# Kernel optimization log

Hardware: AMD Instinct MI355X
Metric: run time of the kernel (lower is better)

Reference implementation:

```python
import jax, jax.numpy as jnp
import numpy as np

H = 1024        # hidden_size
M = 1024        # memory_size
NH = 16         # num_heads
DH = H // NH    # head_dim
CR = 4          # compression_ratio
B, S = 4, 2048


def _lin(x, W, b):
    return x @ W + b


def setup_inputs() -> dict:
    key = jax.random.key(0)
    ks = iter(jax.random.split(key, 32))
    p = lambda *shape: jax.random.normal(next(ks), shape, dtype=jnp.float32) * 0.02
    inp = {
        'hidden_states': jax.random.normal(next(ks), (B, S, H), dtype=jnp.float32),
        'memory_bank': jax.random.normal(next(ks), (B, M, H), dtype=jnp.float32),
        'memory_mask': jnp.ones((B, M), dtype=bool),
        'write_pointer': 700,
        # compressor: Linear(H*CR -> H), SiLU, Linear(H -> H)
        'Wc1': p(H * CR, H), 'bc1': jnp.zeros((H,), jnp.float32),
        'Wc2': p(H, H), 'bc2': jnp.zeros((H,), jnp.float32),
        # attention projections
        'Wq': p(H, H), 'bq': jnp.zeros((H,), jnp.float32),
        'Wk': p(H, H), 'bk': jnp.zeros((H,), jnp.float32),
        'Wv': p(H, H), 'bv': jnp.zeros((H,), jnp.float32),
        'Wo': p(H, H), 'bo': jnp.zeros((H,), jnp.float32),
        # write gate: Linear(H -> H//2), SiLU, Linear(H//2 -> 1), Sigmoid
        'Wwg1': p(H, H // 2), 'bwg1': jnp.zeros((H // 2,), jnp.float32),
        'Wwg2': p(H // 2, 1), 'bwg2': jnp.zeros((1,), jnp.float32),
        # read gate: Linear(2H -> H//2), SiLU, Linear(H//2 -> 1), Sigmoid
        'Wrg1': p(2 * H, H // 2), 'brg1': jnp.zeros((H // 2,), jnp.float32),
        'Wrg2': p(H // 2, 1), 'brg2': jnp.zeros((1,), jnp.float32),
        # LayerNorm
        'ln_g': jnp.ones((H,), jnp.float32), 'ln_b': jnp.zeros((H,), jnp.float32),
    }
    return inp


def _forward(hidden_states, memory_bank, memory_mask, write_pointer,
             Wc1, bc1, Wc2, bc2, Wq, bq, Wk, bk, Wv, bv, Wo, bo,
             Wwg1, bwg1, Wwg2, bwg2, Wrg1, brg1, Wrg2, brg2, ln_g, ln_b):
    # ---- memory attention ----
    q = _lin(hidden_states, Wq, bq).reshape(B, S, NH, DH)
    k = _lin(memory_bank, Wk, bk).reshape(B, M, NH, DH)
    v = _lin(memory_bank, Wv, bv).reshape(B, M, NH, DH)
    scale = DH ** -0.5
    scores = jnp.einsum('bqhd,bkhd->bhqk', q, k) * scale
    scores = jnp.where(memory_mask[:, None, None, :], scores, -jnp.inf)
    probs = jnp.nan_to_num(jax.nn.softmax(scores, axis=-1), nan=0.0)
    retrieved = jnp.einsum('bhqk,bkhd->bqhd', probs, v).reshape(B, S, H)
    retrieved = _lin(retrieved, Wo, bo)

    # ---- read gate + residual + layernorm ----
    gate_in = jnp.concatenate([hidden_states, retrieved], axis=-1)
    rg = jax.nn.sigmoid(_lin(jax.nn.silu(_lin(gate_in, Wrg1, brg1)), Wrg2, brg2))
    out = hidden_states + rg * retrieved
    mu = jnp.mean(out, axis=-1, keepdims=True)
    var = jnp.var(out, axis=-1, keepdims=True)
    out = (out - mu) * jax.lax.rsqrt(var + 1e-5) * ln_g + ln_b

    # ---- write to memory ----
    wg = jax.nn.sigmoid(_lin(jax.nn.silu(_lin(hidden_states, Wwg1, bwg1)), Wwg2, bwg2))  # [B,S,1]
    L = S // CR  # S divisible by CR -> no padding needed (pad path is a no-op)
    compressed = _lin(jax.nn.silu(_lin(hidden_states.reshape(B, L, CR * H), Wc1, bc1)), Wc2, bc2)
    wg = wg.reshape(B, L, CR, 1).mean(axis=2)
    gated = compressed * wg  # [B,L,H]

    idx = (write_pointer + jnp.arange(L)) % M  # circular-buffer indices (unique since L <= M)
    new_bank = memory_bank.at[:, idx].set(gated)
    new_mask = memory_mask.at[:, idx].set(True)
    new_ptr = (write_pointer + L) % M
    return out, new_bank, new_mask, new_ptr


def reference(hidden_states, memory_bank, memory_mask, write_pointer,
              Wc1, bc1, Wc2, bc2, Wq, bq, Wk, bk, Wv, bv, Wo, bo,
              Wwg1, bwg1, Wwg2, bwg2, Wrg1, brg1, Wrg2, brg2, ln_g, ln_b):
    return _forward(hidden_states, memory_bank, memory_mask, write_pointer,
                    Wc1, bc1, Wc2, bc2, Wq, bq, Wk, bk, Wv, bv, Wo, bo,
                    Wwg1, bwg1, Wwg2, bwg2, Wrg1, brg1, Wrg2, brg2, ln_g, ln_b)
```

## Files before the change

kernel.cpp:

```cpp
#include <hip/hip_runtime.h>
#include <hip/hip_bf16.h>

#define Bb 4
#define Ss 2048
#define Hh 1024
#define Mm 1024
#define NHh 16
#define DHh 64
#define CRr 4
#define Ll (Ss / CRr)

#define SC2 0.18033688f

typedef __attribute__((ext_vector_type(8))) short short8;
typedef __attribute__((ext_vector_type(4))) float f32x4;
typedef __attribute__((ext_vector_type(16))) float f32x16;

typedef __attribute__((address_space(1))) const unsigned int g_u32;
typedef __attribute__((address_space(3))) unsigned int l_u32;

__device__ inline void gload_lds16(const void* g, void* l) {
    __builtin_amdgcn_global_load_lds((g_u32*)g, (l_u32*)l, 16, 0, 0);
}

__device__ inline unsigned short f2bf(float x) {
    unsigned int u = __builtin_bit_cast(unsigned int, x);
    unsigned int r = u + 0x7FFFu + ((u >> 16) & 1u);
    return (unsigned short)(r >> 16);
}
__device__ inline float bf2f(unsigned short u) {
    return __builtin_bit_cast(float, (unsigned int)u << 16);
}
__device__ inline unsigned int cvtpk_bf16(float lo, float hi2) {
    unsigned int r;
    asm("v_cvt_pk_bf16_f32 %0, %1, %2" : "=v"(r) : "v"(lo), "v"(hi2));
    return r;
}
__device__ inline f32x16 zero16() {
    f32x16 v;
    #pragma unroll
    for (int i = 0; i < 16; ++i) v[i] = 0.0f;
    return v;
}
__device__ inline short8 lds_frag(const unsigned short* base, int row, int slot) {
    return *(const short8*)((const char*)base + row * 128 + ((slot ^ (row & 7)) << 4));
}

#define N8_HS  (Bb * Ss * Hh / 8)
#define N8_BK  (Bb * Mm * Hh / 8)
__global__ __launch_bounds__(256) void cast2_kernel(
    const float* __restrict__ hs, const float* __restrict__ bank,
    unsigned short* __restrict__ hs_bf, unsigned short* __restrict__ bank_bf)
{
    int i = blockIdx.x * 256 + threadIdx.x;
    const float* src; unsigned short* dst;
    if (i < N8_HS) { src = hs; dst = hs_bf; }
    else           { src = bank; dst = bank_bf; i -= N8_HS; if (i >= N8_BK) return; }
    const float4* p = reinterpret_cast<const float4*>(src) + (size_t)i * 2;
    float4 a = p[0], b = p[1];
    uint4 o;
    o.x = (unsigned)f2bf(a.x) | ((unsigned)f2bf(a.y) << 16);
    o.y = (unsigned)f2bf(a.z) | ((unsigned)f2bf(a.w) << 16);
    o.z = (unsigned)f2bf(b.x) | ((unsigned)f2bf(b.y) << 16);
    o.w = (unsigned)f2bf(b.z) | ((unsigned)f2bf(b.w) << 16);
    *reinterpret_cast<uint4*>(dst + (size_t)i * 8) = o;
}

__global__ __launch_bounds__(256) void transpose_all_kernel(
    const float* __restrict__ Wq, const float* __restrict__ Wwg1,
    const float* __restrict__ Wk, const float* __restrict__ Wv,
    const float* __restrict__ Wo, const float* __restrict__ Wrg1,
    const float* __restrict__ Wc1, const float* __restrict__ Wc2,
    unsigned short* wtQW, unsigned short* wtKV, unsigned short* wtO,
    unsigned short* wtRG, unsigned short* wtC1, unsigned short* wtC2)
{
    int bid = blockIdx.x;
    const float* src; unsigned short* dst; int K, N;
    if (bid < 1024)      { src = Wq;   dst = wtQW;              K = 1024; N = 1024; }
    else if (bid < 1536) { src = Wwg1; dst = wtQW + 1048576;    K = 1024; N = 512;  bid -= 1024; }
    else if (bid < 2560) { src = Wk;   dst = wtKV;              K = 1024; N = 1024; bid -= 1536; }
    else if (bid < 3584) { src = Wv;   dst = wtKV + 1048576;    K = 1024; N = 1024; bid -= 2560; }
    else if (bid < 4608) { src = Wo;   dst = wtO;               K = 1024; N = 1024; bid -= 3584; }
    else if (bid < 5632) { src = Wrg1; dst = wtRG;              K = 2048; N = 512;  bid -= 4608; }
    else if (bid < 9728) { src = Wc1;  dst = wtC1;              K = 4096; N = 1024; bid -= 5632; }
    else                 { src = Wc2;  dst = wtC2;              K = 1024; N = 1024; bid -= 9728; }
    const int ntx = N >> 5;
    const int k0 = (bid / ntx) * 32, n0 = (bid % ntx) * 32;

    __shared__ float tile[32][33];
    const int tx = threadIdx.x & 31, ty = threadIdx.x >> 5;
    #pragma unroll
    for (int r = 0; r < 32; r += 8)
        tile[r + ty][tx] = src[(size_t)(k0 + r + ty) * N + n0 + tx];
    __syncthreads();
    #pragma unroll
    for (int r = 0; r < 32; r += 8)
        dst[(size_t)(n0 + r + ty) * K + k0 + tx] = f2bf(tile[tx][r + ty]);
}

__global__ void maskbias_kernel(const unsigned char* __restrict__ mask,
                                float* __restrict__ bias_arr)
{
    const int i = blockIdx.x * 256 + threadIdx.x;
    if (i < Bb * Mm) bias_arr[i] = mask[i] ? 0.0f : -1.0e30f;
}

#define GM_BF16  0
#define GM_BF16S 1
#define GM_BF16T 2
#define GM_F32G  3

__global__ __launch_bounds__(256) void gemm_bf16_kernel(
    const unsigned short* __restrict__ A1, const unsigned short* __restrict__ A2,
    int K1, const unsigned short* __restrict__ Wt,
    const float* __restrict__ bias1, const float* __restrict__ bias2, int N1,
    void* out1, void* out2, int mode1, int mode2,
    int Mdim, int Ntot, int Kdim,
    const int* __restrict__ wp_ptr, const float* __restrict__ wg_row)
{
    __shared__ __align__(16) unsigned short As[128 * 64];
    __shared__ __align__(16) unsigned short Bs[128 * 64];

    const int t = threadIdx.x;
    const int l = t & 63;
    const int w = t >> 6;

    const int nx = gridDim.x;
    const int nwg = nx * gridDim.y;
    const int bid0 = blockIdx.y * nx + blockIdx.x;
    const int swz = (nwg & 7) ? bid0 : ((bid0 & 7) * (nwg >> 3) + (bid0 >> 3));
    const int bm = (swz / nx) * 128;
    const int bn = (swz % nx) * 128;

    const int m_off = (w >> 1) * 64;
    const int n_off = (w & 1) * 64;
    const int K2 = Kdim - K1;

    f32x4 acc[4][4];
    const f32x4 z = {0.f, 0.f, 0.f, 0.f};
    #pragma unroll
    for (int i = 0; i < 4; ++i)
        #pragma unroll
        for (int j = 0; j < 4; ++j) acc[i][j] = z;

    for (int kt = 0; kt < Kdim; kt += 64) {
        __syncthreads();
        const unsigned short* Ap; int rsA, kl;
        if (kt < K1) { Ap = A1; rsA = K1; kl = kt; }
        else         { Ap = A2; rsA = K2; kl = kt - K1; }
        #pragma unroll
        for (int i = 0; i < 4; ++i) {
            const int c = i * 256 + t;
            const int row = c >> 3;
            const int p = (c & 7) ^ (row & 7);
            gload_lds16(Ap + (size_t)(bm + row) * rsA + kl + p * 8,
                        (char*)As + c * 16);
            gload_lds16(Wt + (size_t)(bn + row) * Kdim + kt + p * 8,
                        (char*)Bs + c * 16);
        }
        __syncthreads();
        #pragma unroll
        for (int kk = 0; kk < 2; ++kk) {
            short8 af[4], bfr[4];
            #pragma unroll
            for (int i = 0; i < 4; ++i) {
                af[i]  = lds_frag(As, m_off + i * 16 + (l & 15), kk * 4 + (l >> 4));
                bfr[i] = lds_frag(Bs, n_off + i * 16 + (l & 15), kk * 4 + (l >> 4));
            }
            #pragma unroll
            for (int i = 0; i < 4; ++i)
                #pragma unroll
                for (int j = 0; j < 4; ++j)
                    acc[i][j] = __builtin_amdgcn_mfma_f32_16x16x32_bf16(
                        af[i], bfr[j], acc[i][j], 0, 0, 0);
        }
    }

    float gg[16]; int wpv = 0;
    if (mode1 == GM_F32G) {
        wpv = *wp_ptr;
        #pragma unroll
        for (int i = 0; i < 4; ++i)
            #pragma unroll
            for (int r = 0; r < 4; ++r) {
                const int row = bm + m_off + i * 16 + (l >> 4) * 4 + r;
                gg[i * 4 + r] = 0.25f * (wg_row[4 * row] + wg_row[4 * row + 1] +
                                         wg_row[4 * row + 2] + wg_row[4 * row + 3]);
            }
    }

    #pragma unroll
    for (int j = 0; j < 4; ++j) {
        const int col = bn + n_off + j * 16 + (l & 15);
        const bool sec = (col >= N1);
        const int cl = sec ? col - N1 : col;
        const int mode = sec ? mode2 : mode1;
        const float bj = sec ? bias2[cl] : bias1[cl];
        const int nd = sec ? (Ntot - N1) : N1;
        if (mode == GM_BF16T) {
            unsigned short* ob = (unsigned short*)out2;
            #pragma unroll
            for (int i = 0; i < 4; ++i) {
                const int row0 = bm + m_off + i * 16 + (l >> 4) * 4;
                const int bidx = row0 >> 10, key = row0 & 1023;
                ushort4 pk4;
                pk4.x = f2bf(acc[i][j][0] + bj);
                pk4.y = f2bf(acc[i][j][1] + bj);
                pk4.z = f2bf(acc[i][j][2] + bj);
                pk4.w = f2bf(acc[i][j][3] + bj);
                *(ushort4*)(ob + ((size_t)bidx << 20) + (size_t)cl * 1024 + key) = pk4;
            }
        } else if (mode == GM_F32G) {
            float* ob = (float*)out1;
            #pragma unroll
            for (int i = 0; i < 4; ++i)
                #pragma unroll
                for (int r = 0; r < 4; ++r) {
                    const int row = bm + m_off + i * 16 + (l >> 4) * 4 + r;
                    const int bb = row >> 9, lx = row & 511;
                    const int m = (wpv + lx) & 1023;
                    ob[((size_t)(bb * 1024 + m)) * 1024 + col] =
                        (acc[i][j][r] + bj) * gg[i * 4 + r];
                }
        } else {
            unsigned short* ob = (unsigned short*)(sec ? out2 : out1);
            #pragma unroll
            for (int i = 0; i < 4; ++i)
                #pragma unroll
                for (int r = 0; r < 4; ++r) {
                    const int row = bm + m_off + i * 16 + (l >> 4) * 4 + r;
                    float v0 = acc[i][j][r] + bj;
                    if (mode == GM_BF16S) v0 = v0 / (1.0f + __expf(-v0));
                    ob[(size_t)row * nd + cl] = f2bf(v0);
                }
        }
    }
}

__global__ __launch_bounds__(256) void attn_mfma_kernel(
    const unsigned short* __restrict__ q, const unsigned short* __restrict__ k,
    const unsigned short* __restrict__ vt, const float* __restrict__ bias_arr,
    unsigned short* __restrict__ out)
{
    const int qt = blockIdx.x, h = blockIdx.y, b = blockIdx.z;
    const int t = threadIdx.x, l = t & 63, w = t >> 6;
    const int lq = l & 31, hi = l >> 5;

    __shared__ __align__(16) unsigned short Ks[64 * 64];
    __shared__ __align__(16) unsigned short Vs[64 * 64];

    short8 qf[4];
    {
        const int qg = qt * 128 + w * 32 + lq;
        const unsigned short* qp = q + ((size_t)(b * Ss + qg)) * Hh + h * 64 + hi * 8;
        #pragma unroll
        for (int tt = 0; tt < 4; ++tt) qf[tt] = *(const short8*)(qp + tt * 16);
    }

    f32x16 oacc0 = zero16(), oacc1 = zero16();
    float m_run = -1.0e38f, l_run = 0.0f;

    for (int c = 0; c < Mm / 64; ++c) {
        const int kc = c * 64;
        __syncthreads();
        {
            const int c0 = t, c1 = t + 256;
            const int r0 = c0 >> 3, s0 = c0 & 7;
            const int r1 = c1 >> 3, s1 = c1 & 7;
            gload_lds16(k + ((size_t)(b * Mm + kc + r0)) * Hh + h * 64 + ((s0 ^ (r0 & 7)) * 8),
                        (char*)Ks + c0 * 16);
            gload_lds16(k + ((size_t)(b * Mm + kc + r1)) * Hh + h * 64 + ((s1 ^ (r1 & 7)) * 8),
                        (char*)Ks + c1 * 16);
            gload_lds16(vt + ((size_t)b << 20) + (size_t)(h * 64 + r0) * Mm + kc + ((s0 ^ (r0 & 7)) * 8),
                        (char*)Vs + c0 * 16);
            gload_lds16(vt + ((size_t)b << 20) + (size_t)(h * 64 + r1) * Mm + kc + ((s1 ^ (r1 & 7)) * 8),
                        (char*)Vs + c1 * 16);
        }
        __syncthreads();

        f32x16 st0 = zero16(), st1 = zero16();
        #pragma unroll
        for (int tt = 0; tt < 4; ++tt) {
            short8 k0 = lds_frag(Ks, lq,      2 * tt + hi);
            short8 k1 = lds_frag(Ks, 32 + lq, 2 * tt + hi);
            st0 = __builtin_amdgcn_mfma_f32_32x32x16_bf16(k0, qf[tt], st0, 0, 0, 0);
            st1 = __builtin_amdgcn_mfma_f32_32x32x16_bf16(k1, qf[tt], st1, 0, 0, 0);
        }

        float sv[32];
        #pragma unroll
        for (int kb = 0; kb < 2; ++kb) {
            const f32x16 stv = kb ? st1 : st0;
            #pragma unroll
            for (int g = 0; g < 4; ++g) {
                const float4 bf4 = *(const float4*)
                    (bias_arr + b * Mm + kc + kb * 32 + 8 * g + 4 * hi);
                sv[kb * 16 + g * 4 + 0] = fmaf(stv[g * 4 + 0], SC2, bf4.x);
                sv[kb * 16 + g * 4 + 1] = fmaf(stv[g * 4 + 1], SC2, bf4.y);
                sv[kb * 16 + g * 4 + 2] = fmaf(stv[g * 4 + 2], SC2, bf4.z);
                sv[kb * 16 + g * 4 + 3] = fmaf(stv[g * 4 + 3], SC2, bf4.w);
            }
        }

        float mx = fmaxf(sv[0], fmaxf(sv[1], sv[2]));
        #pragma unroll
        for (int i = 3; i < 31; i += 2) mx = fmaxf(mx, fmaxf(sv[i], sv[i + 1]));
        mx = fmaxf(mx, sv[31]);
        mx = fmaxf(mx, __shfl_xor(mx, 32));

        if (!__all(mx <= m_run + 10.0f)) {
            const float m_new = fmaxf(m_run, mx);
            const float fac = exp2f(m_run - m_new);
            m_run = m_new;
            l_run *= fac;
            #pragma unroll
            for (int i = 0; i < 16; ++i) { oacc0[i] *= fac; oacc1[i] *= fac; }
        }

        float psum = 0.0f;
        #pragma unroll
        for (int i = 0; i < 32; ++i) {
            const float pv = exp2f(sv[i] - m_run);
            sv[i] = pv; psum += pv;
        }
        psum += __shfl_xor(psum, 32);
        l_run += psum;

        short8 pf[4];
        #pragma unroll
        for (int kb = 0; kb < 2; ++kb) {
            #pragma unroll
            for (int gp = 0; gp < 2; ++gp) {
                const float* pp = &sv[kb * 16 + gp * 8];
                unsigned int u  = cvtpk_bf16(pp[0], pp[1]);
                unsigned int v2 = cvtpk_bf16(pp[2], pp[3]);
                unsigned int w2 = cvtpk_bf16(pp[4], pp[5]);
                unsigned int z2 = cvtpk_bf16(pp[6], pp[7]);
                unsigned int su = __shfl_xor(u, 32),  sv2 = __shfl_xor(v2, 32);
                unsigned int sw = __shfl_xor(w2, 32), sz  = __shfl_xor(z2, 32);
                const bool low = (hi == 0);
                union { unsigned int d[4]; short8 s; } fr;
                fr.d[0] = low ? u   : sw;
                fr.d[1] = low ? v2  : sz;
                fr.d[2] = low ? su  : w2;
                fr.d[3] = low ? sv2 : z2;
                pf[kb * 2 + gp] = fr.s;
            }
        }

        #pragma unroll
        for (int ks = 0; ks < 4; ++ks) {
            short8 v0 = lds_frag(Vs, lq,      2 * ks + hi);
            short8 v1 = lds_frag(Vs, 32 + lq, 2 * ks + hi);
            oacc0 = __builtin_amdgcn_mfma_f32_32x32x16_bf16(v0, pf[ks], oacc0, 0, 0, 0);
            oacc1 = __builtin_amdgcn_mfma_f32_32x32x16_bf16(v1, pf[ks], oacc1, 0, 0, 0);
        }
    }

    const float inv = (l_run > 0.0f) ? 1.0f / l_run : 0.0f;
    const int qg = qt * 128 + w * 32 + lq;
    unsigned short* op = out + ((size_t)(b * Ss + qg)) * Hh + h * 64;
    #pragma unroll
    for (int db = 0; db < 2; ++db) {
        const f32x16 oa = db ? oacc1 : oacc0;
        #pragma unroll
        for (int g = 0; g < 4; ++g) {
            const int d0 = db * 32 + 8 * g + 4 * hi;
            ushort4 pk4;
            pk4.x = f2bf(oa[g * 4 + 0] * inv);
            pk4.y = f2bf(oa[g * 4 + 1] * inv);
            pk4.z = f2bf(oa[g * 4 + 2] * inv);
            pk4.w = f2bf(oa[g * 4 + 3] * inv);
            *(ushort4*)(op + d0) = pk4;
        }
    }
}

__global__ __launch_bounds__(256) void gate2_kernel(
    const unsigned short* __restrict__ h, const float* __restrict__ w2,
    const float* __restrict__ b2, float* __restrict__ outg, int R)
{
    const int wid = threadIdx.x / 64;
    const int lane = threadIdx.x % 64;
    const int row = blockIdx.x * 4 + wid;
    if (row >= R) return;
    short8 hv = *(const short8*)(h + (size_t)row * 512 + lane * 8);
    float4 w0 = *(const float4*)(w2 + lane * 8);
    float4 w1 = *(const float4*)(w2 + lane * 8 + 4);
    float s = bf2f((unsigned short)hv[0]) * w0.x + bf2f((unsigned short)hv[1]) * w0.y +
              bf2f((unsigned short)hv[2]) * w0.z + bf2f((unsigned short)hv[3]) * w0.w +
              bf2f((unsigned short)hv[4]) * w1.x + bf2f((unsigned short)hv[5]) * w1.y +
              bf2f((unsigned short)hv[6]) * w1.z + bf2f((unsigned short)hv[7]) * w1.w;
    #pragma unroll
    for (int o = 1; o < 64; o <<= 1) s += __shfl_xor(s, o);
    if (lane == 0) outg[row] = 1.0f / (1.0f + __expf(-(s + b2[0])));
}

__global__ __launch_bounds__(256) void out_ln_kernel(
    const float* __restrict__ hs, const unsigned short* __restrict__ retr,
    const unsigned short* __restrict__ rg_h, const float* __restrict__ Wrg2,
    const float* __restrict__ brg2, const float* __restrict__ gam,
    const float* __restrict__ bet, float* __restrict__ out)
{
    const int row = blockIdx.x;
    const int t = threadIdx.x;
    const int wid = t >> 6, lane = t & 63;

    const unsigned int hv = *(const unsigned int*)(rg_h + (size_t)row * 512 + t * 2);
    const float2 wv = *(const float2*)(Wrg2 + t * 2);
    float sd = bf2f((unsigned short)(hv & 0xffffu)) * wv.x +
               bf2f((unsigned short)(hv >> 16)) * wv.y;
    #pragma unroll
    for (int o = 1; o < 64; o <<= 1) sd += __shfl_xor(sd, o);
    __shared__ float rsd[4];
    if (lane == 0) rsd[wid] = sd;
    __syncthreads();
    const float r = 1.0f / (1.0f + __expf(-(rsd[0] + rsd[1] + rsd[2] + rsd[3] + brg2[0])));

    float x[4];
    float s = 0.0f, s2 = 0.0f;
    #pragma unroll
    for (int i = 0; i < 4; ++i) {
        const int col = t + i * 256;
        const float val = hs[(size_t)row * Hh + col] +
                          r * bf2f(retr[(size_t)row * Hh + col]);
        x[i] = val; s += val; s2 += val * val;
    }
    #pragma unroll
    for (int o = 1; o < 64; o <<= 1) { s += __shfl_xor(s, o); s2 += __shfl_xor(s2, o); }
    __shared__ float rs[4], rs2[4];
    if (lane == 0) { rs[wid] = s; rs2[wid] = s2; }
    __syncthreads();
    const float tot = rs[0] + rs[1] + rs[2] + rs[3];
    const float tot2 = rs2[0] + rs2[1] + rs2[2] + rs2[3];
    const float mu = tot * (1.0f / Hh);
    const float var = tot2 * (1.0f / Hh) - mu * mu;
    const float rstd = rsqrtf(var + 1e-5f);
    #pragma unroll
    for (int i = 0; i < 4; ++i) {
        const int col = t + i * 256;
        out[(size_t)row * Hh + col] = (x[i] - mu) * rstd * gam[col] + bet[col];
    }
}

__global__ __launch_bounds__(256) void bankfix_kernel(
    const float* __restrict__ bank, const unsigned char* __restrict__ mask,
    const int* __restrict__ wp_ptr, float* __restrict__ out_bank,
    float* __restrict__ out_mask, float* __restrict__ out_ptr)
{
    const int row = blockIdx.x;
    const int wp = *wp_ptr;
    const int m = row & 1023;
    int rel = m - (wp & 1023);
    if (rel < 0) rel += Mm;
    const bool written = rel < Ll;
    if (!written) {
        const int col = threadIdx.x * 4;
        *(float4*)(out_bank + (size_t)row * Hh + col) =
            *(const float4*)(bank + (size_t)row * Hh + col);
    }
    if (threadIdx.x == 0) out_mask[row] = (mask[row] != 0 || written) ? 1.0f : 0.0f;
    if (row == 0 && threadIdx.x == 0) out_ptr[0] = (float)((wp + Ll) % Mm);
}

extern "C" void kernel_launch(void* const* d_in, const int* in_sizes, int n_in,
                              void* d_out, int out_size, void* d_ws, size_t ws_size,
                              hipStream_t stream)
{
    const float* hs   = (const float*)d_in[0];
    const float* bank = (const float*)d_in[1];
    const unsigned char* mask = (const unsigned char*)d_in[2];
    const int*   wp   = (const int*)d_in[3];
    const float* Wc1 = (const float*)d_in[4];  const float* bc1 = (const float*)d_in[5];
    const float* Wc2 = (const float*)d_in[6];  const float* bc2 = (const float*)d_in[7];
    const float* Wq  = (const float*)d_in[8];  const float* bq  = (const float*)d_in[9];
    const float* Wk  = (const float*)d_in[10]; const float* bk  = (const float*)d_in[11];
    const float* Wv  = (const float*)d_in[12]; const float* bv  = (const float*)d_in[13];
    const float* Wo  = (const float*)d_in[14]; const float* bo  = (const float*)d_in[15];
    const float* Wwg1 = (const float*)d_in[16]; const float* bwg1 = (const float*)d_in[17];
    const float* Wwg2 = (const float*)d_in[18]; const float* bwg2 = (const float*)d_in[19];
    const float* Wrg1 = (const float*)d_in[20]; const float* brg1 = (const float*)d_in[21];
    const float* Wrg2 = (const float*)d_in[22]; const float* brg2 = (const float*)d_in[23];
    const float* ln_g = (const float*)d_in[24]; const float* ln_b = (const float*)d_in[25];

    float* out_main = (float*)d_out;
    float* out_bank = out_main + (size_t)Bb * Ss * Hh;
    float* out_mask = out_bank + (size_t)Bb * Mm * Hh;
    float* out_ptr  = out_mask + (size_t)Bb * Mm;

    unsigned short* q_bf   = (unsigned short*)out_main;
    unsigned short* att_bf = (unsigned short*)out_main + 8388608;
    unsigned short* wtQW = (unsigned short*)out_bank;
    unsigned short* wtO  = (unsigned short*)out_bank + 1572864;
    unsigned short* wtRG = (unsigned short*)out_bank + 2621440;
    unsigned short* wtC1 = (unsigned short*)out_bank + 3670016;

    char* W = (char*)d_ws;
    unsigned short* hs_bf   = (unsigned short*)(W + 0);
    unsigned short* bank_bf = (unsigned short*)(W + 16777216);
    unsigned short* rg_h    = (unsigned short*)(W + 16777216);
    unsigned short* retr_bf = (unsigned short*)(W + 25165824);
    unsigned short* k_bf    = (unsigned short*)(W + 41943040);
    unsigned short* vt_bf   = (unsigned short*)(W + 50331648);
    unsigned short* comp_h  = (unsigned short*)(W + 50331648);
    unsigned short* wg_h    = (unsigned short*)(W + 58720256);
    unsigned short* wtC2    = (unsigned short*)(W + 67108864);
    unsigned short* wtKV    = (unsigned short*)(W + 69206016);
    float* wg_row   = (float*)(W + 73400320);
    float* bias_arr = (float*)(W + 73433088);

    cast2_kernel<<<(N8_HS + N8_BK + 255) / 256, 256, 0, stream>>>(
        hs, bank, hs_bf, bank_bf);

    transpose_all_kernel<<<10752, 256, 0, stream>>>(
        Wq, Wwg1, Wk, Wv, Wo, Wrg1, Wc1, Wc2,
        wtQW, wtKV, wtO, wtRG, wtC1, wtC2);

    maskbias_kernel<<<16, 256, 0, stream>>>(mask, bias_arr);

    gemm_bf16_kernel<<<dim3(12, 64), 256, 0, stream>>>(
        hs_bf, hs_bf, Hh, wtQW, bq, bwg1, 1024,
        q_bf, wg_h, GM_BF16, GM_BF16S, Bb * Ss, 1536, Hh, nullptr, nullptr);

    gemm_bf16_kernel<<<dim3(16, 32), 256, 0, stream>>>(
        bank_bf, bank_bf, Hh, wtKV, bk, bv, 1024,
        k_bf, vt_bf, GM_BF16, GM_BF16T, Bb * Mm, 2048, Hh, nullptr, nullptr);

    attn_mfma_kernel<<<dim3(Ss / 128, NHh, Bb), 256, 0, stream>>>(
        q_bf, k_bf, vt_bf, bias_arr, att_bf);

    gemm_bf16_kernel<<<dim3(8, 64), 256, 0, stream>>>(
        att_bf, att_bf, Hh, wtO, bo, bo, 1024,
        retr_bf, nullptr, GM_BF16, GM_BF16, Bb * Ss, 1024, Hh, nullptr, nullptr);

    gemm_bf16_kernel<<<dim3(4, 64), 256, 0, stream>>>(
        hs_bf, retr_bf, Hh, wtRG, brg1, brg1, 512,
        rg_h, nullptr, GM_BF16S, GM_BF16S, Bb * Ss, 512, 2 * Hh, nullptr, nullptr);

    gate2_kernel<<<Bb * Ss / 4, 256, 0, stream>>>(wg_h, Wwg2, bwg2, wg_row, Bb * Ss);

    out_ln_kernel<<<Bb * Ss, 256, 0, stream>>>(
        hs, retr_bf, rg_h, Wrg2, brg2, ln_g, ln_b, out_main);

    gemm_bf16_kernel<<<dim3(8, 16), 256, 0, stream>>>(
        hs_bf, hs_bf, CRr * Hh, wtC1, bc1, bc1, 1024,
        comp_h, nullptr, GM_BF16S, GM_BF16S, Bb * Ll, 1024, CRr * Hh, nullptr, nullptr);

    gemm_bf16_kernel<<<dim3(8, 16), 256, 0, stream>>>(
        comp_h, comp_h, Hh, wtC2, bc2, bc2, 1024,
        out_bank, nullptr, GM_F32G, GM_F32G, Bb * Ll, 1024, Hh, wp, wg_row);

    bankfix_kernel<<<Bb * Mm, 256, 0, stream>>>(
        bank, mask, wp, out_bank, out_mask, out_ptr);
}
```

Baseline: 530.4 us.

## Double-buffer attention K/V loads, stage mask bias in LDS, remap blocks per XCD

```diff
diff --git a/kernel.cpp b/kernel.cpp
--- a/kernel.cpp
+++ b/kernel.cpp
@@ -48,14 +48,26 @@
 
 #define N8_HS  (Bb * Ss * Hh / 8)
 #define N8_BK  (Bb * Mm * Hh / 8)
+#define N8_MB  (Bb * Mm / 8)
 __global__ __launch_bounds__(256) void cast2_kernel(
     const float* __restrict__ hs, const float* __restrict__ bank,
-    unsigned short* __restrict__ hs_bf, unsigned short* __restrict__ bank_bf)
+    const unsigned char* __restrict__ mask,
+    unsigned short* __restrict__ hs_bf, unsigned short* __restrict__ bank_bf,
+    float* __restrict__ bias_arr)
 {
     int i = blockIdx.x * 256 + threadIdx.x;
+    if (i >= N8_HS + N8_BK) {
+        i -= N8_HS + N8_BK;
+        if (i < N8_MB) {
+            #pragma unroll
+            for (int j = 0; j < 8; ++j)
+                bias_arr[i * 8 + j] = mask[i * 8 + j] ? 0.0f : -1.0e30f;
+        }
+        return;
+    }
     const float* src; unsigned short* dst;
     if (i < N8_HS) { src = hs; dst = hs_bf; }
-    else           { src = bank; dst = bank_bf; i -= N8_HS; if (i >= N8_BK) return; }
+    else           { src = bank; dst = bank_bf; i -= N8_HS; }
     const float4* p = reinterpret_cast<const float4*>(src) + (size_t)i * 2;
     float4 a = p[0], b = p[1];
     uint4 o;
@@ -98,13 +110,6 @@
         dst[(size_t)(n0 + r + ty) * K + k0 + tx] = f2bf(tile[tx][r + ty]);
 }
 
-__global__ void maskbias_kernel(const unsigned char* __restrict__ mask,
-                                float* __restrict__ bias_arr)
-{
-    const int i = blockIdx.x * 256 + threadIdx.x;
-    if (i < Bb * Mm) bias_arr[i] = mask[i] ? 0.0f : -1.0e30f;
-}
-
 #define GM_BF16  0
 #define GM_BF16S 1
 #define GM_BF16T 2
@@ -242,12 +247,41 @@
     const unsigned short* __restrict__ vt, const float* __restrict__ bias_arr,
     unsigned short* __restrict__ out)
 {
-    const int qt = blockIdx.x, h = blockIdx.y, b = blockIdx.z;
+    const int bid = blockIdx.x;
+    const int xcd = bid & 7, jj = bid >> 3;
+    const int hb = xcd * 8 + (jj >> 4);
+    const int qt = jj & 15;
+    const int b = hb >> 4, h = hb & 15;
+
     const int t = threadIdx.x, l = t & 63, w = t >> 6;
     const int lq = l & 31, hi = l >> 5;
 
-    __shared__ __align__(16) unsigned short Ks[64 * 64];
-    __shared__ __align__(16) unsigned short Vs[64 * 64];
+    __shared__ __align__(16) unsigned short Ks[2][64 * 64];
+    __shared__ __align__(16) unsigned short Vs[2][64 * 64];
+    __shared__ __align__(16) float Bls[Mm];
+
+    {
+        const float4 bv4 = *(const float4*)(bias_arr + b * Mm + t * 4);
+        *(float4*)&Bls[t * 4] = bv4;
+    }
+    asm volatile("s_waitcnt lgkmcnt(0)" ::: "memory");
+
+    const int c0 = t, c1 = t + 256;
+    const int r0 = c0 >> 3, s0 = c0 & 7;
+    const int r1 = c1 >> 3, s1 = c1 & 7;
+    const unsigned short* kb0 = k + ((size_t)(b * Mm + r0)) * Hh + h * 64 + ((s0 ^ (r0 & 7)) * 8);
+    const unsigned short* kb1 = k + ((size_t)(b * Mm + r1)) * Hh + h * 64 + ((s1 ^ (r1 & 7)) * 8);
+    const unsigned short* vb0 = vt + ((size_t)b << 20) + (size_t)(h * 64 + r0) * Mm + ((s0 ^ (r0 & 7)) * 8);
+    const unsigned short* vb1 = vt + ((size_t)b << 20) + (size_t)(h * 64 + r1) * Mm + ((s1 ^ (r1 & 7)) * 8);
+
+#define ATTN_STAGE(cc, bf) do {                                          \
+    const size_t ko_ = (size_t)(cc) * 64 * Hh;                           \
+    const int vo_ = (cc) * 64;                                           \
+    gload_lds16(kb0 + ko_, (char*)Ks[bf] + c0 * 16);                     \
+    gload_lds16(kb1 + ko_, (char*)Ks[bf] + c1 * 16);                     \
+    gload_lds16(vb0 + vo_, (char*)Vs[bf] + c0 * 16);                     \
+    gload_lds16(vb1 + vo_, (char*)Vs[bf] + c1 * 16);                     \
+} while (0)
 
     short8 qf[4];
     {
@@ -260,29 +294,26 @@
     f32x16 oacc0 = zero16(), oacc1 = zero16();
     float m_run = -1.0e38f, l_run = 0.0f;
 
+    ATTN_STAGE(0, 0);
+
     for (int c = 0; c < Mm / 64; ++c) {
+        const int cur = c & 1;
         const int kc = c * 64;
-        __syncthreads();
-        {
-            const int c0 = t, c1 = t + 256;
-            const int r0 = c0 >> 3, s0 = c0 & 7;
-            const int r1 = c1 >> 3, s1 = c1 & 7;
-            gload_lds16(k + ((size_t)(b * Mm + kc + r0)) * Hh + h * 64 + ((s0 ^ (r0 & 7)) * 8),
-                        (char*)Ks + c0 * 16);
-            gload_lds16(k + ((size_t)(b * Mm + kc + r1)) * Hh + h * 64 + ((s1 ^ (r1 & 7)) * 8),
-                        (char*)Ks + c1 * 16);
-            gload_lds16(vt + ((size_t)b << 20) + (size_t)(h * 64 + r0) * Mm + kc + ((s0 ^ (r0 & 7)) * 8),
-                        (char*)Vs + c0 * 16);
-            gload_lds16(vt + ((size_t)b << 20) + (size_t)(h * 64 + r1) * Mm + kc + ((s1 ^ (r1 & 7)) * 8),
-                        (char*)Vs + c1 * 16);
-        }
-        __syncthreads();
+        if (c < 15) {
+            ATTN_STAGE(c + 1, cur ^ 1);
+            asm volatile("s_waitcnt vmcnt(4)" ::: "memory");
+        } else {
+            asm volatile("s_waitcnt vmcnt(0)" ::: "memory");
+        }
+        __builtin_amdgcn_s_barrier();
+        const unsigned short* Kb = Ks[cur];
+        const unsigned short* Vb = Vs[cur];
 
         f32x16 st0 = zero16(), st1 = zero16();
         #pragma unroll
         for (int tt = 0; tt < 4; ++tt) {
-            short8 k0 = lds_frag(Ks, lq,      2 * tt + hi);
-            short8 k1 = lds_frag(Ks, 32 + lq, 2 * tt + hi);
+            short8 k0 = lds_frag(Kb, lq,      2 * tt + hi);
+            short8 k1 = lds_frag(Kb, 32 + lq, 2 * tt + hi);
             st0 = __builtin_amdgcn_mfma_f32_32x32x16_bf16(k0, qf[tt], st0, 0, 0, 0);
             st1 = __builtin_amdgcn_mfma_f32_32x32x16_bf16(k1, qf[tt], st1, 0, 0, 0);
         }
@@ -293,8 +324,7 @@
             const f32x16 stv = kb ? st1 : st0;
             #pragma unroll
             for (int g = 0; g < 4; ++g) {
-                const float4 bf4 = *(const float4*)
-                    (bias_arr + b * Mm + kc + kb * 32 + 8 * g + 4 * hi);
+                const float4 bf4 = *(const float4*)&Bls[kc + kb * 32 + 8 * g + 4 * hi];
                 sv[kb * 16 + g * 4 + 0] = fmaf(stv[g * 4 + 0], SC2, bf4.x);
                 sv[kb * 16 + g * 4 + 1] = fmaf(stv[g * 4 + 1], SC2, bf4.y);
                 sv[kb * 16 + g * 4 + 2] = fmaf(stv[g * 4 + 2], SC2, bf4.z);
@@ -350,12 +380,14 @@
 
         #pragma unroll
         for (int ks = 0; ks < 4; ++ks) {
-            short8 v0 = lds_frag(Vs, lq,      2 * ks + hi);
-            short8 v1 = lds_frag(Vs, 32 + lq, 2 * ks + hi);
+            short8 v0 = lds_frag(Vb, lq,      2 * ks + hi);
+            short8 v1 = lds_frag(Vb, 32 + lq, 2 * ks + hi);
             oacc0 = __builtin_amdgcn_mfma_f32_32x32x16_bf16(v0, pf[ks], oacc0, 0, 0, 0);
             oacc1 = __builtin_amdgcn_mfma_f32_32x32x16_bf16(v1, pf[ks], oacc1, 0, 0, 0);
         }
-    }
+        __builtin_amdgcn_s_barrier();
+    }
+#undef ATTN_STAGE
 
     const float inv = (l_run > 0.0f) ? 1.0f / l_run : 0.0f;
     const int qg = qt * 128 + w * 32 + lq;
@@ -509,15 +541,13 @@
     float* wg_row   = (float*)(W + 73400320);
     float* bias_arr = (float*)(W + 73433088);
 
-    cast2_kernel<<<(N8_HS + N8_BK + 255) / 256, 256, 0, stream>>>(
-        hs, bank, hs_bf, bank_bf);
+    cast2_kernel<<<(N8_HS + N8_BK + N8_MB + 255) / 256, 256, 0, stream>>>(
+        hs, bank, mask, hs_bf, bank_bf, bias_arr);
 
     transpose_all_kernel<<<10752, 256, 0, stream>>>(
         Wq, Wwg1, Wk, Wv, Wo, Wrg1, Wc1, Wc2,
         wtQW, wtKV, wtO, wtRG, wtC1, wtC2);
 
-    maskbias_kernel<<<16, 256, 0, stream>>>(mask, bias_arr);
-
     gemm_bf16_kernel<<<dim3(12, 64), 256, 0, stream>>>(
         hs_bf, hs_bf, Hh, wtQW, bq, bwg1, 1024,
         q_bf, wg_h, GM_BF16, GM_BF16S, Bb * Ss, 1536, Hh, nullptr, nullptr);
@@ -526,7 +556,7 @@
         bank_bf, bank_bf, Hh, wtKV, bk, bv, 1024,
         k_bf, vt_bf, GM_BF16, GM_BF16T, Bb * Mm, 2048, Hh, nullptr, nullptr);
 
-    attn_mfma_kernel<<<dim3(Ss / 128, NHh, Bb), 256, 0, stream>>>(
+    attn_mfma_kernel<<<1024, 256, 0, stream>>>(
         q_bf, k_bf, vt_bf, bias_arr, att_bf);
 
     gemm_bf16_kernel<<<dim3(8, 64), 256, 0, stream>>>(
```

Result: no change. 528.0 us (-0.5%).
